# Performance work log

Hardware: AMD Instinct MI355X
Metric: run time of the kernel (lower is better)

## Reference

```python
import jax, jax.numpy as jnp
import numpy as np

B, S, D = 1, 2048, 2048
H, DH, DHID, DKER = 16, 128, 128, 64
EPS = 1e-6

def _gelu(x):
    return jax.nn.gelu(x, approximate=False)  # torch F.gelu default is exact erf

def setup_inputs() -> dict:
    key = jax.random.key(0)
    ks = jax.random.split(key, 12)
    inp = {
        'q': jax.random.normal(ks[0], (B, S, D), jnp.float32),
        'k': jax.random.normal(ks[1], (B, S, D), jnp.float32),
        'v': jax.random.normal(ks[2], (B, S, D), jnp.float32),
        'lr_attn_mask': jax.random.randint(ks[3], (1, 1, S, S), 0, 2) > 0,
        'sparse_norms_lse': jax.random.normal(ks[4], (B, H, S, 1), jnp.float32),
        'sparse_attn_weights': jax.random.normal(ks[5], (B, H, S, S), jnp.float32) * 0.1,
        'kernel_q_mat1': jax.random.normal(ks[6], (H, DH, DHID), jnp.float32) * 0.05,
        'kernel_k_mat1': jax.random.normal(ks[7], (H, DH, DHID), jnp.float32) * 0.05,
        'kernel_q_mat2': jax.random.normal(ks[8], (H, DHID, DKER), jnp.float32) * 0.05,
        'kernel_k_mat2': jax.random.normal(ks[9], (H, DHID, DKER), jnp.float32) * 0.05,
        'interaction_k': jax.random.normal(ks[10], (H, DKER, DKER), jnp.float32) * 0.05,
        'scalingD': jnp.ones((1, H, 1, DKER), jnp.float32) * 1e-4,
        'scalingD2': jnp.ones((1, H, 1, DKER), jnp.float32) * 1e-4,
    }
    return inp

def reference(q, k, v, lr_attn_mask, sparse_norms_lse, sparse_attn_weights,
              kernel_q_mat1, kernel_k_mat1, kernel_q_mat2, kernel_k_mat2,
              interaction_k, scalingD, scalingD2):
    b, s, d = q.shape
    dh = d // H
    # [B,S,D] -> [B,H,S,dh]
    q = q.reshape(b, s, H, dh).transpose(0, 2, 1, 3)
    k = k.reshape(b, s, H, dh).transpose(0, 2, 1, 3)
    v = v.reshape(b, s, H, dh).transpose(0, 2, 1, 3)
    # per-head kernel feature maps (dropout is identity, p=0.0)
    q = _gelu(jnp.einsum('bhsd,hde->bhse', q, kernel_q_mat1))
    q = _gelu(jnp.einsum('bhsd,hde->bhse', q, kernel_q_mat2))
    k = _gelu(jnp.einsum('bhsd,hde->bhse', k, kernel_k_mat1))
    k = jnp.abs(scalingD) * _gelu(jnp.einsum('bhsd,hde->bhse', k, kernel_k_mat2))
    k = k + jnp.einsum('bhse,hef->bhsf', k, interaction_k) * scalingD2
    # low-rank kernelized scores: [B,H,S,S]
    out = jnp.einsum('bhse,bhte->bhst', jnp.abs(q), jnp.abs(k))
    mask = lr_attn_mask  # bool, broadcasts over [B,H,S,S]
    out = jnp.where(mask, out, 0.0)
    lr_norms_lse = jnp.log(out.sum(axis=-1, keepdims=True) + EPS)
    norm_factor_lse = jnp.logaddexp(lr_norms_lse, sparse_norms_lse)
    # log-domain merge of low-rank and sparse scores
    out = jnp.where(mask, jnp.log(out + EPS), sparse_attn_weights)
    out = jnp.exp(out - norm_factor_lse)
    out = jnp.einsum('bhst,bhtd->bhsd', out, v)
    return out.transpose(0, 2, 1, 3).reshape(b, s, d)
```

## Files before the change

kernel.cpp:

```cpp
#include <hip/hip_runtime.h>
#include <math.h>

#define S 2048
#define DD 2048
#define NH 16
#define DH 128
#define DHID 128
#define DKER 64
#define EPSF 1e-6f

typedef __attribute__((ext_vector_type(8))) short bf16x8;
typedef __attribute__((ext_vector_type(4))) float f32x4;

__device__ __forceinline__ float gelu_f(float x) {
    return 0.5f * x * (1.0f + erff(x * 0.7071067811865475f));
}

__device__ __forceinline__ ushort f2b(float x) {
    uint32_t u = __float_as_uint(x);
    uint32_t r = (u + 0x7FFFu + ((u >> 16) & 1u)) >> 16;
    return (ushort)r;
}

__device__ __forceinline__ bf16x8 pack8(float4 a, float4 b) {
    bf16x8 r;
    r[0] = (short)f2b(a.x); r[1] = (short)f2b(a.y);
    r[2] = (short)f2b(a.z); r[3] = (short)f2b(a.w);
    r[4] = (short)f2b(b.x); r[5] = (short)f2b(b.y);
    r[6] = (short)f2b(b.z); r[7] = (short)f2b(b.w);
    return r;
}

__device__ __forceinline__ bf16x8 merge8(bf16x8 ps, uint mb, float4 wa, float4 wb) {
    float w[8] = {wa.x, wa.y, wa.z, wa.w, wb.x, wb.y, wb.z, wb.w};
    float p[8];
    #pragma unroll
    for (int j = 0; j < 8; ++j) {
        float sv = __uint_as_float(((uint)(ushort)ps[j]) << 16);
        p[j] = ((mb >> j) & 1) ? (sv + EPSF) : __expf(w[j]);
    }
    return pack8(make_float4(p[0], p[1], p[2], p[3]),
                 make_float4(p[4], p[5], p[6], p[7]));
}

__global__ __launch_bounds__(256) void k_wprep(const float* __restrict__ wq1,
                                               const float* __restrict__ wk1,
                                               const float* __restrict__ wq2,
                                               const float* __restrict__ wk2,
                                               const float* __restrict__ ik,
                                               ushort* __restrict__ w1qt,
                                               ushort* __restrict__ w1kt,
                                               ushort* __restrict__ w2qt,
                                               ushort* __restrict__ w2kt,
                                               ushort* __restrict__ ikt) {
    const int h = blockIdx.x, m = blockIdx.y, tid = threadIdx.x;
    const float* src; ushort* dst; int D;
    if (m == 0)      { src = wq1 + h * 16384; dst = w1qt + h * 16384; D = 128; }
    else if (m == 1) { src = wk1 + h * 16384; dst = w1kt + h * 16384; D = 128; }
    else if (m == 2) { src = wq2 + h * 8192;  dst = w2qt + h * 8192;  D = 128; }
    else if (m == 3) { src = wk2 + h * 8192;  dst = w2kt + h * 8192;  D = 128; }
    else             { src = ik  + h * 4096;  dst = ikt  + h * 4096;  D = 64;  }
    const int E = (m == 0 || m == 1) ? 128 : 64;
    const int dsh = (D == 128) ? 7 : 6;
    const int n = E * D;
    for (int idx = tid; idx < n; idx += 256) {
        int e = idx >> dsh, d = idx & (D - 1);
        dst[idx] = f2b(src[d * E + e]);
    }
}

__global__ __launch_bounds__(256) void k_fused(const float* __restrict__ Xq,
                                               const float* __restrict__ Xk,
                                               const ushort* __restrict__ w1qt,
                                               const ushort* __restrict__ w1kt,
                                               const ushort* __restrict__ w2qt,
                                               const ushort* __restrict__ w2kt,
                                               const ushort* __restrict__ ikt,
                                               const float* __restrict__ sD,
                                               const float* __restrict__ sD2,
                                               ushort* __restrict__ Q2,
                                               ushort* __restrict__ K3) {
    const int h = blockIdx.y;
    const int s0 = blockIdx.x * 64;
    const int z = blockIdx.z;
    const int tid = threadIdx.x;
    const int wv = tid >> 6, lane = tid & 63;
    const int ln = lane & 15, quad = lane >> 4;
    __shared__ ushort Y1s[64][136];
    __shared__ ushort K2s[64][72];

    const float* X = z ? Xk : Xq;
    const ushort* w1t = z ? w1kt : w1qt;
    const ushort* w2t = z ? w2kt : w2qt;

    const float* Xr = X + (size_t)(s0 + wv * 16 + ln) * DD + h * DH;
    bf16x8 a1[4];
    #pragma unroll
    for (int ks = 0; ks < 4; ++ks)
        a1[ks] = pack8(*(const float4*)(Xr + ks * 32 + quad * 8),
                       *(const float4*)(Xr + ks * 32 + quad * 8 + 4));

    const ushort* W1h = w1t + (size_t)h * DH * DHID;
    f32x4 c1[8];
    #pragma unroll
    for (int n = 0; n < 8; ++n) c1[n] = (f32x4){0.f, 0.f, 0.f, 0.f};
    #pragma unroll
    for (int ks = 0; ks < 4; ++ks) {
        bf16x8 bb[8];
        #pragma unroll
        for (int n = 0; n < 8; ++n)
            bb[n] = *(const bf16x8*)(W1h + (size_t)(n * 16 + ln) * DHID +
                                     ks * 32 + quad * 8);
        #pragma unroll
        for (int n = 0; n < 8; ++n)
            c1[n] = __builtin_amdgcn_mfma_f32_16x16x32_bf16(a1[ks], bb[n], c1[n], 0, 0, 0);
    }
    #pragma unroll
    for (int n = 0; n < 8; ++n)
        #pragma unroll
        for (int r = 0; r < 4; ++r)
            Y1s[wv * 16 + quad * 4 + r][n * 16 + ln] = f2b(gelu_f(c1[n][r]));

    bf16x8 a2[4];
    #pragma unroll
    for (int ks = 0; ks < 4; ++ks)
        a2[ks] = *(const bf16x8*)&Y1s[wv * 16 + ln][ks * 32 + quad * 8];
    const ushort* W2h = w2t + (size_t)h * DKER * DHID;
    f32x4 c2[4];
    #pragma unroll
    for (int n = 0; n < 4; ++n) c2[n] = (f32x4){0.f, 0.f, 0.f, 0.f};
    #pragma unroll
    for (int ks = 0; ks < 4; ++ks) {
        bf16x8 bb[4];
        #pragma unroll
        for (int n = 0; n < 4; ++n)
            bb[n] = *(const bf16x8*)(W2h + (size_t)(n * 16 + ln) * DHID +
                                     ks * 32 + quad * 8);
        #pragma unroll
        for (int n = 0; n < 4; ++n)
            c2[n] = __builtin_amdgcn_mfma_f32_16x16x32_bf16(a2[ks], bb[n], c2[n], 0, 0, 0);
    }

    if (z == 0) {
        #pragma unroll
        for (int n = 0; n < 4; ++n)
            #pragma unroll
            for (int r = 0; r < 4; ++r)
                Q2[((size_t)h * S + s0 + wv * 16 + quad * 4 + r) * DKER + n * 16 + ln] =
                    f2b(fabsf(gelu_f(c2[n][r])));
        return;
    }

    float k2v[4][4];
    float sdv[4], sd2v[4];
    #pragma unroll
    for (int n = 0; n < 4; ++n) {
        sdv[n]  = fabsf(sD[h * DKER + n * 16 + ln]);
        sd2v[n] = sD2[h * DKER + n * 16 + ln];
    }
    #pragma unroll
    for (int n = 0; n < 4; ++n)
        #pragma unroll
        for (int r = 0; r < 4; ++r) {
            k2v[n][r] = sdv[n] * gelu_f(c2[n][r]);
            K2s[wv * 16 + quad * 4 + r][n * 16 + ln] = f2b(k2v[n][r]);
        }
    bf16x8 a3[2];
    #pragma unroll
    for (int ks = 0; ks < 2; ++ks)
        a3[ks] = *(const bf16x8*)&K2s[wv * 16 + ln][ks * 32 + quad * 8];
    const ushort* Ikh = ikt + (size_t)h * DKER * DKER;
    f32x4 c3[4];
    #pragma unroll
    for (int n = 0; n < 4; ++n) c3[n] = (f32x4){0.f, 0.f, 0.f, 0.f};
    #pragma unroll
    for (int ks = 0; ks < 2; ++ks) {
        bf16x8 bb[4];
        #pragma unroll
        for (int n = 0; n < 4; ++n)
            bb[n] = *(const bf16x8*)(Ikh + (size_t)(n * 16 + ln) * DKER +
                                     ks * 32 + quad * 8);
        #pragma unroll
        for (int n = 0; n < 4; ++n)
            c3[n] = __builtin_amdgcn_mfma_f32_16x16x32_bf16(a3[ks], bb[n], c3[n], 0, 0, 0);
    }
    #pragma unroll
    for (int n = 0; n < 4; ++n)
        #pragma unroll
        for (int r = 0; r < 4; ++r)
            K3[((size_t)h * S + s0 + wv * 16 + quad * 4 + r) * DKER + n * 16 + ln] =
                f2b(fabsf(k2v[n][r] + c3[n][r] * sd2v[n]));
}

__global__ __launch_bounds__(256) void k_vt(const float* __restrict__ V,
                                            ushort* __restrict__ Vt) {
    const int h = blockIdx.y;
    const int t0 = blockIdx.x * 64;
    const int tid = threadIdx.x;
    __shared__ ushort Ls[128][72];
    #pragma unroll
    for (int it = 0; it < 8; ++it) {
        int idx = it * 256 + tid;
        int r = idx >> 5, c4 = idx & 31;
        float4 v = *(const float4*)(V + (size_t)(t0 + r) * DD + h * DH + c4 * 4);
        Ls[c4 * 4 + 0][r] = f2b(v.x);
        Ls[c4 * 4 + 1][r] = f2b(v.y);
        Ls[c4 * 4 + 2][r] = f2b(v.z);
        Ls[c4 * 4 + 3][r] = f2b(v.w);
    }
    __syncthreads();
    #pragma unroll
    for (int it = 0; it < 4; ++it) {
        int idx = it * 256 + tid;
        int row = idx >> 3, cc = idx & 7;
        *(bf16x8*)(Vt + ((size_t)h * DH + row) * S + t0 + cc * 8) =
            *(const bf16x8*)(&Ls[row][cc * 8]);
    }
}

__global__ __launch_bounds__(256) void k_mpack(const int* __restrict__ mask,
                                               uint* __restrict__ pm) {
    const int gw = blockIdx.x * 4 + (threadIdx.x >> 6);
    const int lane = threadIdx.x & 63;
    const int row = gw >> 5;
    const int w64 = gw & 31;
    int mv = mask[(size_t)row * S + w64 * 64 + lane];
    unsigned long long b = __ballot(mv != 0);
    if (lane == 0)  pm[row * 64 + w64 * 2]     = (uint)b;
    if (lane == 32) pm[row * 64 + w64 * 2 + 1] = (uint)(b >> 32);
}

__global__ __launch_bounds__(256, 2) void k_attn(const ushort* __restrict__ Q2,
                                                 const ushort* __restrict__ K3,
                                                 const ushort* __restrict__ Vt,
                                                 const uint* __restrict__ pm,
                                                 const float* __restrict__ Wsp,
                                                 const float* __restrict__ lse,
                                                 float* __restrict__ out) {
    const int bid = blockIdx.x;
    const int id = (bid & 7) * 64 + (bid >> 3);
    const int h = id >> 5;
    const int s0 = (id & 31) * 64;
    const int tid = threadIdx.x;
    const int wv = tid >> 6, lane = tid & 63;
    const int ln = lane & 15, quad = lane >> 4;
    __shared__ ushort K3s[64][72];
    __shared__ ushort Vts[128][72];
    __shared__ ushort Ps[4][16][72];

    const ushort* K3h = K3 + (size_t)h * S * DKER;
    const ushort* Vth = Vt + (size_t)h * DH * S;
    const int srow_q = s0 + wv * 16 + quad * 4;
    const int arow   = s0 + wv * 16 + ln;
    const int rk = tid >> 3, ck = tid & 7;

    const float* Wr = Wsp + (size_t)h * S * S + (size_t)arow * S;
    const uint*  pr = pm + (size_t)arow * 64;

    bf16x8 aq[2];
    #pragma unroll
    for (int ks = 0; ks < 2; ++ks)
        aq[ks] = *(const bf16x8*)(Q2 + ((size_t)h * S + arow) * DKER +
                                  ks * 32 + quad * 8);

    f32x4 O[8];
    #pragma unroll
    for (int v = 0; v < 8; ++v) O[v] = (f32x4){0.f, 0.f, 0.f, 0.f};
    float rs[4] = {0.f, 0.f, 0.f, 0.f};

    bf16x8 sk[2][2], sv[2][4];
    uint2  mw[2][4];
    float4 wbuf[2][4];
    uint2  mwa[2];

#define PREF_W(T, SL) do {                                                         \
    if ((T) < 32) {                                                                \
        const float* wp_ = Wr + (T) * 64 + quad * 8;                               \
        wbuf[SL][0] = *(const float4*)wp_;                                         \
        wbuf[SL][1] = *(const float4*)(wp_ + 4);                                   \
        wbuf[SL][2] = *(const float4*)(wp_ + 32);                                  \
        wbuf[SL][3] = *(const float4*)(wp_ + 36);                                  \
        mwa[SL] = *(const uint2*)(pr + (T) * 2);                                   \
    }                                                                              \
} while (0)

#define PREF_KV(T, P) do {                                                         \
    if ((T) < 32) {                                                                \
        const int t0_ = (T) * 64;                                                  \
        _Pragma("unroll") for (int c_ = 0; c_ < 2; ++c_)                           \
            sk[P][c_] = *(const bf16x8*)(K3h +                                     \
                (size_t)(t0_ + rk + c_ * 32) * DKER + ck * 8);                     \
        _Pragma("unroll") for (int c_ = 0; c_ < 4; ++c_)                           \
            sv[P][c_] = *(const bf16x8*)(Vth +                                     \
                (size_t)(rk + c_ * 32) * S + t0_ + ck * 8);                        \
        _Pragma("unroll") for (int r_ = 0; r_ < 4; ++r_)                           \
            mw[P][r_] = *(const uint2*)(pm + (size_t)(srow_q + r_) * 64 +          \
                                        (T) * 2);                                  \
    }                                                                              \
} while (0)

#define STEP(T, P, PN) do {                                                        \
    __syncthreads();                                 \
    _Pragma("unroll") for (int c_ = 0; c_ < 2; ++c_)                               \
        *(bf16x8*)&K3s[rk + c_ * 32][ck * 8] = sk[P][c_];                          \
    _Pragma("unroll") for (int c_ = 0; c_ < 4; ++c_)                               \
        *(bf16x8*)&Vts[rk + c_ * 32][ck * 8] = sv[P][c_];                          \
    __syncthreads();                                      \
    PREF_KV((T) + 1, PN);                                                          \
    f32x4 sc[4];                                                                   \
    _Pragma("unroll") for (int n_ = 0; n_ < 4; ++n_)                               \
        sc[n_] = (f32x4){0.f, 0.f, 0.f, 0.f};                                      \
    _Pragma("unroll") for (int ks_ = 0; ks_ < 2; ++ks_)                            \
    _Pragma("unroll") for (int n_ = 0; n_ < 4; ++n_) {                             \
        bf16x8 bf = *(const bf16x8*)&K3s[n_ * 16 + ln][ks_ * 32 + quad * 8];       \
        sc[n_] = __builtin_amdgcn_mfma_f32_16x16x32_bf16(aq[ks_], bf, sc[n_],      \
                                                         0, 0, 0);                  \
    }                                                                              \
    _Pragma("unroll") for (int n_ = 0; n_ < 4; ++n_)                               \
    _Pragma("unroll") for (int r_ = 0; r_ < 4; ++r_) {                             \
        uint word = (n_ >= 2) ? mw[P][r_].y : mw[P][r_].x;                         \
        int m_ = (word >> (((n_ & 1) << 4) + ln)) & 1;                             \
        float s_ = sc[n_][r_];                                                     \
        if (m_) rs[r_] += s_;                                                      \
        Ps[wv][quad * 4 + r_][n_ * 16 + ln] = f2b(s_);                             \
    }                                                                              \
                \
    bf16x8 pa0, pa1;                                                               \
    {                                                                              \
        bf16x8 ps0 = *(const bf16x8*)&Ps[wv][ln][quad * 8];                        \
        bf16x8 ps1 = *(const bf16x8*)&Ps[wv][ln][32 + quad * 8];                   \
        uint2 ma_ = mwa[(T) & 1];                                                  \
        pa0 = merge8(ps0, ma_.x >> (quad * 8), wbuf[(T) & 1][0],                   \
                     wbuf[(T) & 1][1]);                                            \
        pa1 = merge8(ps1, ma_.y >> (quad * 8), wbuf[(T) & 1][2],                   \
                     wbuf[(T) & 1][3]);                                            \
    }                                                                              \
    PREF_W((T) + 2, (T) & 1);                   \
    _Pragma("unroll") for (int v_ = 0; v_ < 8; ++v_) {                             \
        bf16x8 vf = *(const bf16x8*)&Vts[v_ * 16 + ln][quad * 8];                  \
        O[v_] = __builtin_amdgcn_mfma_f32_16x16x32_bf16(pa0, vf, O[v_], 0, 0, 0);  \
    }                                                                              \
    _Pragma("unroll") for (int v_ = 0; v_ < 8; ++v_) {                             \
        bf16x8 vf = *(const bf16x8*)&Vts[v_ * 16 + ln][32 + quad * 8];             \
        O[v_] = __builtin_amdgcn_mfma_f32_16x16x32_bf16(pa1, vf, O[v_], 0, 0, 0);  \
    }                                                                              \
} while (0)

    PREF_W(0, 0);
    PREF_W(1, 1);
    PREF_KV(0, 0);
    for (int it = 0; it < 32; it += 2) {
        STEP(it, 0, 1);
        STEP(it + 1, 1, 0);
    }
#undef PREF_W
#undef PREF_KV
#undef STEP

    #pragma unroll
    for (int r = 0; r < 4; ++r) {
        float v = rs[r];
        v += __shfl_xor(v, 1); v += __shfl_xor(v, 2);
        v += __shfl_xor(v, 4); v += __shfl_xor(v, 8);
        rs[r] = v;
    }
    float idv[4];
    #pragma unroll
    for (int r = 0; r < 4; ++r)
        idv[r] = 1.f / (rs[r] + EPSF + expf(lse[(size_t)h * S + srow_q + r]));
    #pragma unroll
    for (int v = 0; v < 8; ++v)
        #pragma unroll
        for (int r = 0; r < 4; ++r)
            out[(size_t)(srow_q + r) * DD + h * DH + v * 16 + ln] = O[v][r] * idv[r];
}

extern "C" void kernel_launch(void* const* d_in, const int* in_sizes, int n_in,
                              void* d_out, int out_size, void* d_ws, size_t ws_size,
                              hipStream_t stream) {
    const float* q   = (const float*)d_in[0];
    const float* k   = (const float*)d_in[1];
    const float* v   = (const float*)d_in[2];
    const int*   msk = (const int*)d_in[3];
    const float* lse = (const float*)d_in[4];
    const float* spw = (const float*)d_in[5];
    const float* wq1 = (const float*)d_in[6];
    const float* wk1 = (const float*)d_in[7];
    const float* wq2 = (const float*)d_in[8];
    const float* wk2 = (const float*)d_in[9];
    const float* ik  = (const float*)d_in[10];
    const float* sD  = (const float*)d_in[11];
    const float* sD2 = (const float*)d_in[12];
    float* out = (float*)d_out;

    ushort* q2b  = (ushort*)d_ws;
    ushort* k3b  = q2b + (size_t)NH * S * DKER;
    ushort* vt   = k3b + (size_t)NH * S * DKER;
    uint*   pm   = (uint*)(vt + (size_t)NH * DH * S);
    ushort* w1qt = (ushort*)(pm + (size_t)S * 64);
    ushort* w1kt = w1qt + (size_t)NH * DH * DHID;
    ushort* w2qt = w1kt + (size_t)NH * DH * DHID;
    ushort* w2kt = w2qt + (size_t)NH * DKER * DHID;
    ushort* ikt  = w2kt + (size_t)NH * DKER * DHID;

    dim3 g(S / 64, NH), b(256);
    k_wprep<<<dim3(NH, 5), b, 0, stream>>>(wq1, wk1, wq2, wk2, ik,
                                           w1qt, w1kt, w2qt, w2kt, ikt);
    k_mpack<<<dim3(S * 32 / 4), b, 0, stream>>>(msk, pm);
    k_vt<<<g, b, 0, stream>>>(v, vt);
    k_fused<<<dim3(S / 64, NH, 2), b, 0, stream>>>(q, k, w1qt, w1kt, w2qt, w2kt,
                                                   ikt, sD, sD2, q2b, k3b);
    k_attn<<<dim3(512), b, 0, stream>>>(q2b, k3b, vt, pm, spw, lse, out);
}
```

Baseline: 501.7 us.

## Stream K, V, sparse weights and mask into LDS via direct global-to-LDS loads

```diff
diff --git a/kernel.cpp b/kernel.cpp
--- a/kernel.cpp
+++ b/kernel.cpp
@@ -31,16 +31,25 @@
     return r;
 }
 
-__device__ __forceinline__ bf16x8 merge8(bf16x8 ps, uint mb, float4 wa, float4 wb) {
-    float w[8] = {wa.x, wa.y, wa.z, wa.w, wb.x, wb.y, wb.z, wb.w};
-    float p[8];
+__device__ __forceinline__ bf16x8 merge8(bf16x8 ps, uint mb, f32x4 wa, f32x4 wb) {
+    float w[8] = {wa[0], wa[1], wa[2], wa[3], wb[0], wb[1], wb[2], wb[3]};
+    bf16x8 r;
     #pragma unroll
     for (int j = 0; j < 8; ++j) {
         float sv = __uint_as_float(((uint)(ushort)ps[j]) << 16);
-        p[j] = ((mb >> j) & 1) ? (sv + EPSF) : __expf(w[j]);
-    }
-    return pack8(make_float4(p[0], p[1], p[2], p[3]),
-                 make_float4(p[4], p[5], p[6], p[7]));
+        float p = ((mb >> j) & 1) ? (sv + EPSF) : __expf(w[j]);
+        r[j] = (short)f2b(p);
+    }
+    return r;
+}
+
+__device__ __forceinline__ void gl16(const void* g, void* l) {
+    __builtin_amdgcn_global_load_lds((const __attribute__((address_space(1))) uint*)g,
+                                     (__attribute__((address_space(3))) uint*)l, 16, 0, 0);
+}
+__device__ __forceinline__ void gl4(const void* g, void* l) {
+    __builtin_amdgcn_global_load_lds((const __attribute__((address_space(1))) uint*)g,
+                                     (__attribute__((address_space(3))) uint*)l, 4, 0, 0);
 }
 
 __global__ __launch_bounds__(256) void k_wprep(const float* __restrict__ wq1,
@@ -244,18 +253,25 @@
     const int tid = threadIdx.x;
     const int wv = tid >> 6, lane = tid & 63;
     const int ln = lane & 15, quad = lane >> 4;
-    __shared__ ushort K3s[64][72];
-    __shared__ ushort Vts[128][72];
-    __shared__ ushort Ps[4][16][72];
+
+    __shared__ ushort Ks[2][32][64];
+    __shared__ ushort Vs[2][128][32];
+    __shared__ float  Ws[2][64][32];
+    __shared__ uint   Ms[2][64];
+    __shared__ ushort Ps[4][16][40];
 
     const ushort* K3h = K3 + (size_t)h * S * DKER;
     const ushort* Vth = Vt + (size_t)h * DH * S;
+    const float*  Wh  = Wsp + (size_t)h * S * S;
     const int srow_q = s0 + wv * 16 + quad * 4;
     const int arow   = s0 + wv * 16 + ln;
-    const int rk = tid >> 3, ck = tid & 7;
-
-    const float* Wr = Wsp + (size_t)h * S * S + (size_t)arow * S;
-    const uint*  pr = pm + (size_t)arow * 64;
+
+    const int kR = wv * 8 + (lane >> 3);
+    const int kC = ((lane & 7) ^ ((lane >> 3) & 7)) * 8;
+    const int vR = wv * 32 + (lane >> 2);
+    const int vC = ((lane & 3) ^ ((lane >> 2) & 3)) * 8;
+    const int wR = wv * 16 + (lane >> 3);
+    const int wC = ((lane & 7) ^ ((lane >> 3) & 7)) * 4;
 
     bf16x8 aq[2];
     #pragma unroll
@@ -268,94 +284,68 @@
     for (int v = 0; v < 8; ++v) O[v] = (f32x4){0.f, 0.f, 0.f, 0.f};
     float rs[4] = {0.f, 0.f, 0.f, 0.f};
 
-    bf16x8 sk[2][2], sv[2][4];
-    uint2  mw[2][4];
-    float4 wbuf[2][4];
-    uint2  mwa[2];
-
-#define PREF_W(T, SL) do {                                                         \
-    if ((T) < 32) {                                                                \
-        const float* wp_ = Wr + (T) * 64 + quad * 8;                               \
-        wbuf[SL][0] = *(const float4*)wp_;                                         \
-        wbuf[SL][1] = *(const float4*)(wp_ + 4);                                   \
-        wbuf[SL][2] = *(const float4*)(wp_ + 32);                                  \
-        wbuf[SL][3] = *(const float4*)(wp_ + 36);                                  \
-        mwa[SL] = *(const uint2*)(pr + (T) * 2);                                   \
-    }                                                                              \
+#define STAGE(T, B) do {                                                           \
+    const int t0_ = (T) * 32;                                                      \
+    gl16(K3h + (size_t)(t0_ + kR) * DKER + kC, &Ks[B][wv * 8][0]);                 \
+    gl16(Vth + (size_t)vR * S + t0_ + vC, &Vs[B][wv * 32][0]);                     \
+    gl16(Vth + (size_t)(vR + 16) * S + t0_ + vC, &Vs[B][wv * 32 + 16][0]);         \
+    gl16(Wh + (size_t)(s0 + wR) * S + t0_ + wC, &Ws[B][wv * 16][0]);               \
+    gl16(Wh + (size_t)(s0 + wR + 8) * S + t0_ + wC, &Ws[B][wv * 16 + 8][0]);       \
+    if (wv == 0) gl4(pm + (size_t)(s0 + lane) * 64 + (T), &Ms[B][0]);              \
 } while (0)
 
-#define PREF_KV(T, P) do {                                                         \
-    if ((T) < 32) {                                                                \
-        const int t0_ = (T) * 64;                                                  \
-        _Pragma("unroll") for (int c_ = 0; c_ < 2; ++c_)                           \
-            sk[P][c_] = *(const bf16x8*)(K3h +                                     \
-                (size_t)(t0_ + rk + c_ * 32) * DKER + ck * 8);                     \
-        _Pragma("unroll") for (int c_ = 0; c_ < 4; ++c_)                           \
-            sv[P][c_] = *(const bf16x8*)(Vth +                                     \
-                (size_t)(rk + c_ * 32) * S + t0_ + ck * 8);                        \
-        _Pragma("unroll") for (int r_ = 0; r_ < 4; ++r_)                           \
-            mw[P][r_] = *(const uint2*)(pm + (size_t)(srow_q + r_) * 64 +          \
-                                        (T) * 2);                                  \
-    }                                                                              \
-} while (0)
-
-#define STEP(T, P, PN) do {                                                        \
-    __syncthreads();                                 \
-    _Pragma("unroll") for (int c_ = 0; c_ < 2; ++c_)                               \
-        *(bf16x8*)&K3s[rk + c_ * 32][ck * 8] = sk[P][c_];                          \
-    _Pragma("unroll") for (int c_ = 0; c_ < 4; ++c_)                               \
-        *(bf16x8*)&Vts[rk + c_ * 32][ck * 8] = sv[P][c_];                          \
-    __syncthreads();                                      \
-    PREF_KV((T) + 1, PN);                                                          \
-    f32x4 sc[4];                                                                   \
-    _Pragma("unroll") for (int n_ = 0; n_ < 4; ++n_)                               \
-        sc[n_] = (f32x4){0.f, 0.f, 0.f, 0.f};                                      \
+#define COMPUTE(B) do {                                                            \
+    f32x4 sc[2];                                                                   \
+    sc[0] = (f32x4){0.f, 0.f, 0.f, 0.f};                                           \
+    sc[1] = (f32x4){0.f, 0.f, 0.f, 0.f};                                           \
     _Pragma("unroll") for (int ks_ = 0; ks_ < 2; ++ks_)                            \
-    _Pragma("unroll") for (int n_ = 0; n_ < 4; ++n_) {                             \
-        bf16x8 bf = *(const bf16x8*)&K3s[n_ * 16 + ln][ks_ * 32 + quad * 8];       \
+    _Pragma("unroll") for (int n_ = 0; n_ < 2; ++n_) {                             \
+        bf16x8 bf = *(const bf16x8*)&Ks[B][n_ * 16 + ln]                           \
+                                       [((ks_ * 4 + quad) ^ (ln & 7)) * 8];        \
         sc[n_] = __builtin_amdgcn_mfma_f32_16x16x32_bf16(aq[ks_], bf, sc[n_],      \
                                                          0, 0, 0);                  \
     }                                                                              \
-    _Pragma("unroll") for (int n_ = 0; n_ < 4; ++n_)                               \
+    uint mwq[4];                                                                   \
+    _Pragma("unroll") for (int r_ = 0; r_ < 4; ++r_)                               \
+        mwq[r_] = Ms[B][wv * 16 + quad * 4 + r_];                                  \
+    _Pragma("unroll") for (int n_ = 0; n_ < 2; ++n_)                               \
     _Pragma("unroll") for (int r_ = 0; r_ < 4; ++r_) {                             \
-        uint word = (n_ >= 2) ? mw[P][r_].y : mw[P][r_].x;                         \
-        int m_ = (word >> (((n_ & 1) << 4) + ln)) & 1;                             \
+        int m_ = (mwq[r_] >> (n_ * 16 + ln)) & 1;                                  \
         float s_ = sc[n_][r_];                                                     \
         if (m_) rs[r_] += s_;                                                      \
         Ps[wv][quad * 4 + r_][n_ * 16 + ln] = f2b(s_);                             \
     }                                                                              \
-                \
-    bf16x8 pa0, pa1;                                                               \
-    {                                                                              \
-        bf16x8 ps0 = *(const bf16x8*)&Ps[wv][ln][quad * 8];                        \
-        bf16x8 ps1 = *(const bf16x8*)&Ps[wv][ln][32 + quad * 8];                   \
-        uint2 ma_ = mwa[(T) & 1];                                                  \
-        pa0 = merge8(ps0, ma_.x >> (quad * 8), wbuf[(T) & 1][0],                   \
-                     wbuf[(T) & 1][1]);                                            \
-        pa1 = merge8(ps1, ma_.y >> (quad * 8), wbuf[(T) & 1][2],                   \
-                     wbuf[(T) & 1][3]);                                            \
-    }                                                                              \
-    PREF_W((T) + 2, (T) & 1);                   \
+    uint mwa = Ms[B][wv * 16 + ln];                                                \
+    bf16x8 ps = *(const bf16x8*)&Ps[wv][ln][quad * 8];                             \
+    f32x4 w0 = *(const f32x4*)&Ws[B][wv * 16 + ln][((quad * 2) ^ (ln & 7)) * 4];   \
+    f32x4 w1 = *(const f32x4*)&Ws[B][wv * 16 + ln]                                 \
+                                 [((quad * 2 + 1) ^ (ln & 7)) * 4];                \
+    bf16x8 pa = merge8(ps, mwa >> (quad * 8), w0, w1);                             \
     _Pragma("unroll") for (int v_ = 0; v_ < 8; ++v_) {                             \
-        bf16x8 vf = *(const bf16x8*)&Vts[v_ * 16 + ln][quad * 8];                  \
-        O[v_] = __builtin_amdgcn_mfma_f32_16x16x32_bf16(pa0, vf, O[v_], 0, 0, 0);  \
-    }                                                                              \
-    _Pragma("unroll") for (int v_ = 0; v_ < 8; ++v_) {                             \
-        bf16x8 vf = *(const bf16x8*)&Vts[v_ * 16 + ln][32 + quad * 8];             \
-        O[v_] = __builtin_amdgcn_mfma_f32_16x16x32_bf16(pa1, vf, O[v_], 0, 0, 0);  \
+        bf16x8 vf = *(const bf16x8*)&Vs[B][v_ * 16 + ln][(quad ^ (ln & 3)) * 8];   \
+        O[v_] = __builtin_amdgcn_mfma_f32_16x16x32_bf16(pa, vf, O[v_], 0, 0, 0);   \
     }                                                                              \
 } while (0)
 
-    PREF_W(0, 0);
-    PREF_W(1, 1);
-    PREF_KV(0, 0);
-    for (int it = 0; it < 32; it += 2) {
-        STEP(it, 0, 1);
-        STEP(it + 1, 1, 0);
-    }
-#undef PREF_W
-#undef PREF_KV
-#undef STEP
+    STAGE(0, 0);
+    for (int t = 0; t < 63; ++t) {
+        const int bc = t & 1, bn = bc ^ 1;
+        STAGE(t + 1, bn);
+        if (wv == 0) asm volatile("s_waitcnt vmcnt(6)" ::: "memory");
+        else         asm volatile("s_waitcnt vmcnt(5)" ::: "memory");
+        __builtin_amdgcn_s_barrier();
+        asm volatile("" ::: "memory");
+        COMPUTE(bc);
+        asm volatile("" ::: "memory");
+        __builtin_amdgcn_s_barrier();
+        asm volatile("" ::: "memory");
+    }
+    asm volatile("s_waitcnt vmcnt(0)" ::: "memory");
+    __builtin_amdgcn_s_barrier();
+    asm volatile("" ::: "memory");
+    COMPUTE(1);
+#undef STAGE
+#undef COMPUTE
 
     #pragma unroll
     for (int r = 0; r < 4; ++r) {
```

After: 505.0 us. No clear change (+0.7%).
